# Performance work log

Hardware: AMD Instinct MI355X
Metric: run time of the kernel (lower is better)

Reference implementation:

```python
import jax, jax.numpy as jnp
import numpy as np
import math

NUM_BUCKETS = 32
MAX_DISTANCE = 128
NUM_HEADS = 16
D_MODEL = 1024
HEAD_DIM = D_MODEL // NUM_HEADS


def _relative_position_bucket(relative_position, num_buckets=NUM_BUCKETS, max_distance=MAX_DISTANCE):
    # bidirectional=False path of the original
    rp = -jnp.minimum(relative_position, 0)  # non-negative distances
    max_exact = num_buckets // 2
    is_small = rp < max_exact
    rp_safe = jnp.maximum(rp, 1).astype(jnp.float32)
    rp_if_large = max_exact + (
        jnp.log(rp_safe / max_exact) / math.log(max_distance / max_exact) * (num_buckets - max_exact)
    ).astype(jnp.int32)
    rp_if_large = jnp.minimum(rp_if_large, num_buckets - 1)
    return jnp.where(is_small, rp, rp_if_large)


def relative_bias(rab_weight, q_len, k_len):
    ctx = jnp.arange(q_len)[:, None]
    mem = jnp.arange(k_len)[None, :]
    buckets = _relative_position_bucket(mem - ctx)  # [Q, K]
    vals = rab_weight[buckets]                       # [Q, K, H]
    return jnp.transpose(vals, (2, 0, 1))[None]      # [1, H, Q, K]


def setup_inputs() -> dict:
    key = jax.random.key(0)
    k1, k2, k3, k4 = jax.random.split(key, 4)
    B, S = 4, 2048
    return {
        "v": jax.random.normal(k1, (B, S, D_MODEL), dtype=jnp.float32),
        "k": jax.random.normal(k2, (B, S, D_MODEL), dtype=jnp.float32),
        "q": jax.random.normal(k3, (B, S, D_MODEL), dtype=jnp.float32),
        "rab_weight": jax.random.normal(k4, (NUM_BUCKETS, NUM_HEADS), dtype=jnp.float32),
    }


def reference(v, k, q, rab_weight):
    B, S, _ = q.shape
    def split(x):
        return jnp.transpose(x.reshape(B, S, NUM_HEADS, HEAD_DIM), (0, 2, 1, 3))  # [B,H,S,D]
    qh, kh, vh = split(q), split(k), split(v)
    scores = jnp.einsum("bhqd,bhkd->bhqk", qh, kh)          # [B,H,S,S]
    scores = scores + relative_bias(rab_weight, S, S)        # add relative bias
    av = jnp.einsum("bhqk,bhkd->bhqd", jax.nn.silu(scores), vh)
    return jnp.transpose(av, (0, 2, 1, 3)).reshape(B, S, D_MODEL)
```

## Files before the change

### kernel.cpp

```cpp
#include <hip/hip_runtime.h>

#define NB 4
#define SEQ 2048
#define NH 16
#define HD 64
#define DMODEL 1024

typedef short bf16x8 __attribute__((ext_vector_type(8)));
typedef float f32x16 __attribute__((ext_vector_type(16)));

union FragU {
    bf16x8 v;
    uint2 u2[2];
    unsigned int w[4];
    unsigned short s[8];
};

#if __has_builtin(__builtin_amdgcn_cvt_pk_bf16_f32)
typedef __bf16 v2bf_t __attribute__((ext_vector_type(2)));
__device__ __forceinline__ unsigned int pack_bf16(float lo, float hi) {
    union { v2bf_t h; unsigned int u; } cv;
    cv.h = __builtin_amdgcn_cvt_pk_bf16_f32(lo, hi);
    return cv.u;
}
#else
__device__ __forceinline__ unsigned int pack_bf16(float lo, float hi) {
    unsigned int a = __float_as_uint(lo) + 0x8000u;
    unsigned int b = __float_as_uint(hi) + 0x8000u;
    return __builtin_amdgcn_perm(b, a, 0x07060302);
}
#endif

#define EXP_SCALE 1.44269504f
#define LN2       0.69314718f

__global__ __launch_bounds__(512, 4)
void paa_kernel(const float* __restrict__ Vg, const float* __restrict__ Kg,
                const float* __restrict__ Qg, const float* __restrict__ RW,
                float* __restrict__ Og)
{
    __shared__ __align__(16) unsigned short KsLds[64 * 68];
    __shared__ __align__(16) unsigned short VtLds[64 * 68];
    __shared__ float btab[128];

    const int tid  = threadIdx.x;
    const int lane = tid & 63;
    const int wave = tid >> 6;
    const int half = lane >> 5;
    const int l31  = lane & 31;

    const int bid  = blockIdx.x;
    const int bh   = bid & 63;
    const int qt   = bid >> 6;
    const int b    = bh >> 4;
    const int head = bh & 15;

    const int q0w = qt * 256 + wave * 32;

    if (tid < 128) {
        int rp = tid;
        int bucket;
        if (rp < 16) bucket = rp;
        else {
            int big = 16 + (int)(logf((float)rp * 0.0625f) * 7.6943736f);
            bucket = big < 31 ? big : 31;
        }
        btab[tid] = RW[bucket * NH + head] * EXP_SCALE;
    }

    FragU qf[4];
    {
        const float* qrow = Qg + (size_t)(b * SEQ + q0w + l31) * DMODEL + head * HD;
        #pragma unroll
        for (int kf = 0; kf < 4; ++kf) {
            int dd = kf * 16 + half * 8;
            float4 x0 = *(const float4*)(qrow + dd);
            float4 x1 = *(const float4*)(qrow + dd + 4);
            FragU f;
            f.w[0] = pack_bf16(x0.x * EXP_SCALE, x0.y * EXP_SCALE);
            f.w[1] = pack_bf16(x0.z * EXP_SCALE, x0.w * EXP_SCALE);
            f.w[2] = pack_bf16(x1.x * EXP_SCALE, x1.y * EXP_SCALE);
            f.w[3] = pack_bf16(x1.z * EXP_SCALE, x1.w * EXP_SCALE);
            qf[kf] = f;
        }
    }

    f32x16 oacc[2];
    #pragma unroll
    for (int n = 0; n < 2; ++n)
        #pragma unroll
        for (int r = 0; r < 16; ++r) oacc[n][r] = 0.0f;

    __syncthreads();
    const float bias_d0  = btab[0];
    const float bias_far = btab[127];

    const int krow = tid >> 4;
    const int c4   = tid & 15;
    const int kc2  = tid >> 4;
    const int d4   = tid & 15;

    const float* kbase = Kg + (size_t)(b * SEQ) * DMODEL + head * HD;
    const float* vbase = Vg + (size_t)(b * SEQ) * DMODEL + head * HD;

    for (int it = 0; it < 32; ++it) {
        const int kcb = it * 64;

        #pragma unroll
        for (int i = 0; i < 2; ++i) {
            int row = krow + i * 32;
            float4 x = *(const float4*)(kbase + (size_t)(kcb + row) * DMODEL + c4 * 4);
            uint2 w;
            w.x = pack_bf16(x.x, x.y);
            w.y = pack_bf16(x.z, x.w);
            *(uint2*)&KsLds[row * 68 + c4 * 4] = w;
        }
        {
            const float* vrow = vbase + (size_t)(kcb + kc2 * 2) * DMODEL + d4 * 4;
            float4 x0 = *(const float4*)(vrow);
            float4 x1 = *(const float4*)(vrow + DMODEL);
            *(unsigned int*)&VtLds[(d4 * 4 + 0) * 68 + kc2 * 2] = pack_bf16(x0.x, x1.x);
            *(unsigned int*)&VtLds[(d4 * 4 + 1) * 68 + kc2 * 2] = pack_bf16(x0.y, x1.y);
            *(unsigned int*)&VtLds[(d4 * 4 + 2) * 68 + kc2 * 2] = pack_bf16(x0.z, x1.z);
            *(unsigned int*)&VtLds[(d4 * 4 + 3) * 68 + kc2 * 2] = pack_bf16(x0.w, x1.w);
        }
        __syncthreads();

        FragU pf[4];
        #pragma unroll
        for (int t = 0; t < 2; ++t) {
            const int kcmin = kcb + t * 32;
            FragU ka[4];
            #pragma unroll
            for (int kf = 0; kf < 4; ++kf) {
                int off = (t * 32 + l31) * 68 + kf * 16 + half * 8;
                ka[kf].u2[0] = *(const uint2*)&KsLds[off];
                ka[kf].u2[1] = *(const uint2*)&KsLds[off + 4];
            }
            f32x16 st;
            if (q0w + 31 - kcmin <= 0) {
                #pragma unroll
                for (int r = 0; r < 16; ++r) st[r] = bias_d0;
            } else if (q0w - (kcmin + 31) >= 113) {
                #pragma unroll
                for (int r = 0; r < 16; ++r) st[r] = bias_far;
            } else {
                const int dql = q0w + l31 - kcmin - 4 * half;
                #pragma unroll
                for (int r = 0; r < 16; ++r) {
                    int dv = dql - ((r & 3) + 8 * (r >> 2));
                    dv = dv < 0 ? 0 : (dv > 127 ? 127 : dv);
                    st[r] = btab[dv];
                }
            }
            #pragma unroll
            for (int kf = 0; kf < 4; ++kf)
                st = __builtin_amdgcn_mfma_f32_32x32x16_bf16(ka[kf].v, qf[kf].v, st, 0, 0, 0);

            float vals[16];
            #pragma unroll
            for (int r = 0; r < 16; ++r) {
                float x = st[r];
                float e = __builtin_amdgcn_exp2f(-x);
                vals[r] = x * __builtin_amdgcn_rcpf(1.0f + e);
            }
            #pragma unroll
            for (int j = 0; j < 4; ++j)
                pf[t * 2].w[j]     = pack_bf16(vals[2 * j], vals[2 * j + 1]);
            #pragma unroll
            for (int j = 0; j < 4; ++j)
                pf[t * 2 + 1].w[j] = pack_bf16(vals[8 + 2 * j], vals[9 + 2 * j]);
        }

        #pragma unroll
        for (int f = 0; f < 4; ++f) {
            #pragma unroll
            for (int n = 0; n < 2; ++n) {
                FragU vf;
                int off = (n * 32 + l31) * 68 + f * 16 + half * 4;
                vf.u2[0] = *(const uint2*)&VtLds[off];
                vf.u2[1] = *(const uint2*)&VtLds[off + 8];
                oacc[n] = __builtin_amdgcn_mfma_f32_32x32x16_bf16(pf[f].v, vf.v, oacc[n], 0, 0, 0);
            }
        }
        __syncthreads();
    }

    float* obase = Og + (size_t)(b * SEQ) * DMODEL + head * HD;
    #pragma unroll
    for (int r = 0; r < 16; ++r) {
        int q = q0w + (r & 3) + 8 * (r >> 2) + 4 * half;
        float* orow = obase + (size_t)q * DMODEL;
        #pragma unroll
        for (int n = 0; n < 2; ++n)
            orow[n * 32 + l31] = oacc[n][r] * LN2;
    }
}

extern "C" void kernel_launch(void* const* d_in, const int* in_sizes, int n_in,
                              void* d_out, int out_size, void* d_ws, size_t ws_size,
                              hipStream_t stream) {
    const float* v  = (const float*)d_in[0];
    const float* k  = (const float*)d_in[1];
    const float* q  = (const float*)d_in[2];
    const float* rw = (const float*)d_in[3];
    float* out = (float*)d_out;
    paa_kernel<<<dim3(512), dim3(512), 0, stream>>>(v, k, q, rw, out);
}
```

Before: 220.4 us.

## Double-buffer K/V LDS tiles with register prefetch of next tile

Splits the block so half the threads stage K and half stage V, then prefetches the next 64-row K/V tile into registers before computing on the current LDS buffer. The prefetched tile is converted and written into the other LDS buffer after compute, which leaves one barrier per iteration instead of two. The aim is to hide global load latency behind the MFMA and SiLU work. In exchange it doubles LDS use, adds prefetch registers under the 512x4 launch bounds, and changes the V transpose store pattern.

```diff
diff --git a/kernel.cpp b/kernel.cpp
--- a/kernel.cpp
+++ b/kernel.cpp
@@ -39,8 +39,8 @@
                 const float* __restrict__ Qg, const float* __restrict__ RW,
                 float* __restrict__ Og)
 {
-    __shared__ __align__(16) unsigned short KsLds[64 * 68];
-    __shared__ __align__(16) unsigned short VtLds[64 * 68];
+    __shared__ __align__(16) unsigned short KsLds[2][64 * 68];
+    __shared__ __align__(16) unsigned short VtLds[2][64 * 68];
     __shared__ float btab[128];
 
     const int tid  = threadIdx.x;
@@ -91,40 +91,65 @@
         #pragma unroll
         for (int r = 0; r < 16; ++r) oacc[n][r] = 0.0f;
 
+    const int st_idx = tid & 255;
+    const bool isK   = tid < 256;
+    const int srow   = st_idx >> 4;
+    const int scol   = st_idx & 15;
+    const float* sbase = (isK ? Kg : Vg) + (size_t)(b * SEQ) * DMODEL + head * HD;
+
+    float4 pre[4];
+    if (isK) {
+        #pragma unroll
+        for (int i = 0; i < 4; ++i)
+            pre[i] = *(const float4*)(sbase + (size_t)(srow + i * 16) * DMODEL + scol * 4);
+    } else {
+        #pragma unroll
+        for (int r = 0; r < 4; ++r)
+            pre[r] = *(const float4*)(sbase + (size_t)(srow * 4 + r) * DMODEL + scol * 4);
+    }
     __syncthreads();
     const float bias_d0  = btab[0];
     const float bias_far = btab[127];
 
-    const int krow = tid >> 4;
-    const int c4   = tid & 15;
-    const int kc2  = tid >> 4;
-    const int d4   = tid & 15;
-
-    const float* kbase = Kg + (size_t)(b * SEQ) * DMODEL + head * HD;
-    const float* vbase = Vg + (size_t)(b * SEQ) * DMODEL + head * HD;
+    {
+        const float* pf32 = (const float*)pre;
+        if (isK) {
+            #pragma unroll
+            for (int i = 0; i < 4; ++i) {
+                uint2 w;
+                w.x = pack_bf16(pre[i].x, pre[i].y);
+                w.y = pack_bf16(pre[i].z, pre[i].w);
+                *(uint2*)&KsLds[0][(srow + i * 16) * 68 + scol * 4] = w;
+            }
+        } else {
+            #pragma unroll
+            for (int c = 0; c < 4; ++c) {
+                uint2 w;
+                w.x = pack_bf16(pf32[0 * 4 + c], pf32[1 * 4 + c]);
+                w.y = pack_bf16(pf32[2 * 4 + c], pf32[3 * 4 + c]);
+                *(uint2*)&VtLds[0][(scol * 4 + c) * 68 + srow * 4] = w;
+            }
+        }
+    }
+    __syncthreads();
 
     for (int it = 0; it < 32; ++it) {
         const int kcb = it * 64;
-
-        #pragma unroll
-        for (int i = 0; i < 2; ++i) {
-            int row = krow + i * 32;
-            float4 x = *(const float4*)(kbase + (size_t)(kcb + row) * DMODEL + c4 * 4);
-            uint2 w;
-            w.x = pack_bf16(x.x, x.y);
-            w.y = pack_bf16(x.z, x.w);
-            *(uint2*)&KsLds[row * 68 + c4 * 4] = w;
-        }
-        {
-            const float* vrow = vbase + (size_t)(kcb + kc2 * 2) * DMODEL + d4 * 4;
-            float4 x0 = *(const float4*)(vrow);
-            float4 x1 = *(const float4*)(vrow + DMODEL);
-            *(unsigned int*)&VtLds[(d4 * 4 + 0) * 68 + kc2 * 2] = pack_bf16(x0.x, x1.x);
-            *(unsigned int*)&VtLds[(d4 * 4 + 1) * 68 + kc2 * 2] = pack_bf16(x0.y, x1.y);
-            *(unsigned int*)&VtLds[(d4 * 4 + 2) * 68 + kc2 * 2] = pack_bf16(x0.z, x1.z);
-            *(unsigned int*)&VtLds[(d4 * 4 + 3) * 68 + kc2 * 2] = pack_bf16(x0.w, x1.w);
-        }
-        __syncthreads();
+        const int cur = it & 1;
+        const int nxt = cur ^ 1;
+
+        if (it < 31) {
+            const float* nb = sbase + (size_t)(kcb + 64) * DMODEL;
+            if (isK) {
+                #pragma unroll
+                for (int i = 0; i < 4; ++i)
+                    pre[i] = *(const float4*)(nb + (size_t)(srow + i * 16) * DMODEL + scol * 4);
+            } else {
+                #pragma unroll
+                for (int r = 0; r < 4; ++r)
+                    pre[r] = *(const float4*)(nb + (size_t)(srow * 4 + r) * DMODEL + scol * 4);
+            }
+        }
 
         FragU pf[4];
         #pragma unroll
@@ -134,8 +159,8 @@
             #pragma unroll
             for (int kf = 0; kf < 4; ++kf) {
                 int off = (t * 32 + l31) * 68 + kf * 16 + half * 8;
-                ka[kf].u2[0] = *(const uint2*)&KsLds[off];
-                ka[kf].u2[1] = *(const uint2*)&KsLds[off + 4];
+                ka[kf].u2[0] = *(const uint2*)&KsLds[cur][off];
+                ka[kf].u2[1] = *(const uint2*)&KsLds[cur][off + 4];
             }
             f32x16 st;
             if (q0w + 31 - kcmin <= 0) {
@@ -178,12 +203,33 @@
             for (int n = 0; n < 2; ++n) {
                 FragU vf;
                 int off = (n * 32 + l31) * 68 + f * 16 + half * 4;
-                vf.u2[0] = *(const uint2*)&VtLds[off];
-                vf.u2[1] = *(const uint2*)&VtLds[off + 8];
+                vf.u2[0] = *(const uint2*)&VtLds[cur][off];
+                vf.u2[1] = *(const uint2*)&VtLds[cur][off + 8];
                 oacc[n] = __builtin_amdgcn_mfma_f32_32x32x16_bf16(pf[f].v, vf.v, oacc[n], 0, 0, 0);
             }
         }
-        __syncthreads();
+
+        if (it < 31) {
+            const float* pf32 = (const float*)pre;
+            if (isK) {
+                #pragma unroll
+                for (int i = 0; i < 4; ++i) {
+                    uint2 w;
+                    w.x = pack_bf16(pre[i].x, pre[i].y);
+                    w.y = pack_bf16(pre[i].z, pre[i].w);
+                    *(uint2*)&KsLds[nxt][(srow + i * 16) * 68 + scol * 4] = w;
+                }
+            } else {
+                #pragma unroll
+                for (int c = 0; c < 4; ++c) {
+                    uint2 w;
+                    w.x = pack_bf16(pf32[0 * 4 + c], pf32[1 * 4 + c]);
+                    w.y = pack_bf16(pf32[2 * 4 + c], pf32[3 * 4 + c]);
+                    *(uint2*)&VtLds[nxt][(scol * 4 + c) * 68 + srow * 4] = w;
+                }
+            }
+            __syncthreads();
+        }
     }
 
     float* obase = Og + (size_t)(b * SEQ) * DMODEL + head * HD;
```

New measurement: 475.0 us. 116% more time.

## Pre-convert K/V to swizzled bf16 workspace and stream tiles via LDS DMA

Applied to the files above, without the earlier changes.

Adds a prep kernel that converts K and V to bf16 once, writing K row tiles and transposed V tiles into a workspace in an XOR-swizzled layout. Previously every query-tile block re-read and re-converted the same fp32 K/V. The main kernel now uses global_load_lds to copy 8KB tiles directly into double-buffered LDS, overlapping the next tile's load with compute, and reads fragments with 128-bit swizzled LDS loads. The tile-case branch is also made wave-uniform via readfirstlane. The cost is an extra kernel launch and a workspace round trip, plus a dependence on the DMA timing relative to the barriers.

```diff
diff --git a/kernel.cpp b/kernel.cpp
--- a/kernel.cpp
+++ b/kernel.cpp
@@ -1,6 +1,5 @@
 #include <hip/hip_runtime.h>
 
-#define NB 4
 #define SEQ 2048
 #define NH 16
 #define HD 64
@@ -11,6 +10,7 @@
 
 union FragU {
     bf16x8 v;
+    uint4 u4;
     uint2 u2[2];
     unsigned int w[4];
     unsigned short s[8];
@@ -31,16 +31,73 @@
 }
 #endif
 
+typedef __attribute__((address_space(1))) const unsigned int glob_u32;
+typedef __attribute__((address_space(3))) unsigned int lds_u32;
+__device__ __forceinline__ void dma16(const unsigned short* g, unsigned short* l) {
+    __builtin_amdgcn_global_load_lds((glob_u32*)g, (lds_u32*)l, 16, 0, 0);
+}
+
 #define EXP_SCALE 1.44269504f
 #define LN2       0.69314718f
 
+__global__ __launch_bounds__(256)
+void prep_kernel(const float* __restrict__ Kg, const float* __restrict__ Vg,
+                 unsigned short* __restrict__ wsK, unsigned short* __restrict__ wsVt)
+{
+    __shared__ unsigned short T[64 * 68];
+    const int tid = threadIdx.x;
+    const int blk = blockIdx.x;
+    const int bh  = blk >> 5;
+    const int it  = blk & 31;
+    const int b = bh >> 4, h = bh & 15;
+    const size_t inbase = (size_t)(b * SEQ + it * 64) * DMODEL + h * HD;
+
+    #pragma unroll
+    for (int i = 0; i < 2; ++i) {
+        int item = tid + i * 256;
+        int row = item >> 3, g = item & 7;
+        const float* src = Kg + inbase + (size_t)row * DMODEL + g * 8;
+        float4 x0 = *(const float4*)src;
+        float4 x1 = *(const float4*)(src + 4);
+        uint4 w;
+        w.x = pack_bf16(x0.x, x0.y); w.y = pack_bf16(x0.z, x0.w);
+        w.z = pack_bf16(x1.x, x1.y); w.w = pack_bf16(x1.z, x1.w);
+        size_t dst = (size_t)(bh * 2048 + it * 64 + row) * 64 + ((g ^ (row & 7)) * 8);
+        *(uint4*)&wsK[dst] = w;
+    }
+    {
+        const int kc4 = tid >> 4, d4 = tid & 15;
+        float4 a[4];
+        #pragma unroll
+        for (int r = 0; r < 4; ++r)
+            a[r] = *(const float4*)(Vg + inbase + (size_t)(kc4 * 4 + r) * DMODEL + d4 * 4);
+        const float* af = (const float*)a;
+        #pragma unroll
+        for (int c = 0; c < 4; ++c) {
+            *(unsigned int*)&T[(d4 * 4 + c) * 68 + kc4 * 4]     = pack_bf16(af[0 * 4 + c], af[1 * 4 + c]);
+            *(unsigned int*)&T[(d4 * 4 + c) * 68 + kc4 * 4 + 2] = pack_bf16(af[2 * 4 + c], af[3 * 4 + c]);
+        }
+    }
+    __syncthreads();
+    #pragma unroll
+    for (int i = 0; i < 2; ++i) {
+        int item = tid + i * 256;
+        int d = item >> 3, g = item & 7;
+        uint2 lo = *(const uint2*)&T[d * 68 + g * 8];
+        uint2 hi = *(const uint2*)&T[d * 68 + g * 8 + 4];
+        uint4 w; w.x = lo.x; w.y = lo.y; w.z = hi.x; w.w = hi.y;
+        size_t dst = (size_t)(bh * 32 + it) * 4096 + d * 64 + ((g ^ (d & 7)) * 8);
+        *(uint4*)&wsVt[dst] = w;
+    }
+}
+
 __global__ __launch_bounds__(512, 4)
-void paa_kernel(const float* __restrict__ Vg, const float* __restrict__ Kg,
-                const float* __restrict__ Qg, const float* __restrict__ RW,
-                float* __restrict__ Og)
+void paa_main(const unsigned short* __restrict__ wsK, const unsigned short* __restrict__ wsVt,
+              const float* __restrict__ Qg, const float* __restrict__ RW,
+              float* __restrict__ Og)
 {
-    __shared__ __align__(16) unsigned short KsLds[64 * 68];
-    __shared__ __align__(16) unsigned short VtLds[64 * 68];
+    __shared__ __align__(16) unsigned short KsT[2 * 4096];
+    __shared__ __align__(16) unsigned short VtT[2 * 4096];
     __shared__ float btab[128];
 
     const int tid  = threadIdx.x;
@@ -48,14 +105,14 @@
     const int wave = tid >> 6;
     const int half = lane >> 5;
     const int l31  = lane & 31;
+    const int c7   = l31 & 7;
 
     const int bid  = blockIdx.x;
     const int bh   = bid & 63;
     const int qt   = bid >> 6;
     const int b    = bh >> 4;
     const int head = bh & 15;
-
-    const int q0w = qt * 256 + wave * 32;
+    const int q0w  = qt * 256 + wave * 32;
 
     if (tid < 128) {
         int rp = tid;
@@ -67,6 +124,12 @@
         }
         btab[tid] = RW[bucket * NH + head] * EXP_SCALE;
     }
+
+    const unsigned short* kIt = wsK  + (size_t)bh * 131072 + wave * 512 + lane * 8;
+    const unsigned short* vIt = wsVt + (size_t)bh * 131072 + wave * 512 + lane * 8;
+
+    dma16(kIt, &KsT[wave * 512]);
+    dma16(vIt, &VtT[wave * 512]);
 
     FragU qf[4];
     {
@@ -95,37 +158,13 @@
     const float bias_d0  = btab[0];
     const float bias_far = btab[127];
 
-    const int krow = tid >> 4;
-    const int c4   = tid & 15;
-    const int kc2  = tid >> 4;
-    const int d4   = tid & 15;
-
-    const float* kbase = Kg + (size_t)(b * SEQ) * DMODEL + head * HD;
-    const float* vbase = Vg + (size_t)(b * SEQ) * DMODEL + head * HD;
-
-    for (int it = 0; it < 32; ++it) {
+    const int kaP = l31 * 64 + c7 * 8;
+    const int vfP = l31 * 64 + c7 * 8 + half * 4;
+
+    auto compute_tile = [&](const int BUF, const int it) {
         const int kcb = it * 64;
-
-        #pragma unroll
-        for (int i = 0; i < 2; ++i) {
-            int row = krow + i * 32;
-            float4 x = *(const float4*)(kbase + (size_t)(kcb + row) * DMODEL + c4 * 4);
-            uint2 w;
-            w.x = pack_bf16(x.x, x.y);
-            w.y = pack_bf16(x.z, x.w);
-            *(uint2*)&KsLds[row * 68 + c4 * 4] = w;
-        }
-        {
-            const float* vrow = vbase + (size_t)(kcb + kc2 * 2) * DMODEL + d4 * 4;
-            float4 x0 = *(const float4*)(vrow);
-            float4 x1 = *(const float4*)(vrow + DMODEL);
-            *(unsigned int*)&VtLds[(d4 * 4 + 0) * 68 + kc2 * 2] = pack_bf16(x0.x, x1.x);
-            *(unsigned int*)&VtLds[(d4 * 4 + 1) * 68 + kc2 * 2] = pack_bf16(x0.y, x1.y);
-            *(unsigned int*)&VtLds[(d4 * 4 + 2) * 68 + kc2 * 2] = pack_bf16(x0.z, x1.z);
-            *(unsigned int*)&VtLds[(d4 * 4 + 3) * 68 + kc2 * 2] = pack_bf16(x0.w, x1.w);
-        }
-        __syncthreads();
-
+        const unsigned short* kb = &KsT[BUF * 4096];
+        const unsigned short* vb = &VtT[BUF * 4096];
         FragU pf[4];
         #pragma unroll
         for (int t = 0; t < 2; ++t) {
@@ -133,15 +172,16 @@
             FragU ka[4];
             #pragma unroll
             for (int kf = 0; kf < 4; ++kf) {
-                int off = (t * 32 + l31) * 68 + kf * 16 + half * 8;
-                ka[kf].u2[0] = *(const uint2*)&KsLds[off];
-                ka[kf].u2[1] = *(const uint2*)&KsLds[off + 4];
-            }
+                int g8 = (2 * kf + half) * 8;
+                ka[kf].u4 = *(const uint4*)&kb[t * 2048 + (kaP ^ g8)];
+            }
+            int tcase = (q0w + 31 <= kcmin) ? 0 : ((q0w - (kcmin + 31) >= 113) ? 1 : 2);
+            tcase = __builtin_amdgcn_readfirstlane(tcase);
             f32x16 st;
-            if (q0w + 31 - kcmin <= 0) {
+            if (tcase == 0) {
                 #pragma unroll
                 for (int r = 0; r < 16; ++r) st[r] = bias_d0;
-            } else if (q0w - (kcmin + 31) >= 113) {
+            } else if (tcase == 1) {
                 #pragma unroll
                 for (int r = 0; r < 16; ++r) st[r] = bias_far;
             } else {
@@ -177,12 +217,27 @@
             #pragma unroll
             for (int n = 0; n < 2; ++n) {
                 FragU vf;
-                int off = (n * 32 + l31) * 68 + f * 16 + half * 4;
-                vf.u2[0] = *(const uint2*)&VtLds[off];
-                vf.u2[1] = *(const uint2*)&VtLds[off + 8];
+                const int base = n * 2048;
+                vf.u2[0] = *(const uint2*)&vb[base + (vfP ^ (2 * f * 8))];
+                vf.u2[1] = *(const uint2*)&vb[base + (vfP ^ ((2 * f + 1) * 8))];
                 oacc[n] = __builtin_amdgcn_mfma_f32_32x32x16_bf16(pf[f].v, vf.v, oacc[n], 0, 0, 0);
             }
         }
+    };
+
+    for (int it2 = 0; it2 < 16; ++it2) {
+        const int it = it2 * 2;
+        kIt += 4096; vIt += 4096;
+        dma16(kIt, &KsT[4096 + wave * 512]);
+        dma16(vIt, &VtT[4096 + wave * 512]);
+        compute_tile(0, it);
+        __syncthreads();
+        if (it2 < 15) {
+            kIt += 4096; vIt += 4096;
+            dma16(kIt, &KsT[wave * 512]);
+            dma16(vIt, &VtT[wave * 512]);
+        }
+        compute_tile(1, it + 1);
         __syncthreads();
     }
 
@@ -205,5 +260,8 @@
     const float* q  = (const float*)d_in[2];
     const float* rw = (const float*)d_in[3];
     float* out = (float*)d_out;
-    paa_kernel<<<dim3(512), dim3(512), 0, stream>>>(v, k, q, rw, out);
-}
+    unsigned short* wsK  = (unsigned short*)d_ws;
+    unsigned short* wsVt = wsK + (size_t)4 * NH * SEQ * HD;
+    prep_kernel<<<dim3(2048), dim3(256), 0, stream>>>(k, v, wsK, wsVt);
+    paa_main<<<dim3(512), dim3(512), 0, stream>>>(wsK, wsVt, q, rw, out);
+}
```

New measurement: 231.7 us. 1.05x slower.
